# Kernel tuning notes

Measured on AMD Instinct MI355X. Metric: run time of the kernel, lower is better.

The kernel has to match this reference:

```python
import jax, jax.numpy as jnp
import numpy as np

NUM_BANDS = 12
D_MODEL = 128
NUM_HEADS = 2
HEAD_DIM = D_MODEL // NUM_HEADS


def setup_inputs() -> dict:
    key = jax.random.key(0)
    ks = jax.random.split(key, 12)
    d, B = D_MODEL, NUM_BANDS
    return {
        "x": jax.random.normal(ks[0], (4, 128, 128, B), dtype=jnp.float32),
        "w_embed": jax.random.normal(ks[1], (d,), dtype=jnp.float32) * 0.05,
        "b_embed": jax.random.normal(ks[2], (d,), dtype=jnp.float32) * 0.05,
        "band_pos": jax.random.normal(ks[3], (B, d), dtype=jnp.float32) * 0.02,
        "Wq": jax.random.normal(ks[4], (d, d), dtype=jnp.float32) * (1.0 / np.sqrt(d)),
        "bq": jax.random.normal(ks[5], (d,), dtype=jnp.float32) * 0.02,
        "Wk": jax.random.normal(ks[6], (d, d), dtype=jnp.float32) * (1.0 / np.sqrt(d)),
        "bk": jax.random.normal(ks[7], (d,), dtype=jnp.float32) * 0.02,
        "Wv": jax.random.normal(ks[8], (d, d), dtype=jnp.float32) * (1.0 / np.sqrt(d)),
        "bv": jax.random.normal(ks[9], (d,), dtype=jnp.float32) * 0.02,
        # out_proj is zero-init in the module; use tiny random values so the
        # output is numerically non-trivial for kernel correctness checks.
        "Wo": jax.random.normal(ks[10], (1, d), dtype=jnp.float32) * 0.02,
        "bo": jax.random.normal(ks[11], (1,), dtype=jnp.float32) * 0.02,
    }


def reference(x, w_embed, b_embed, band_pos, Wq, bq, Wk, bk, Wv, bv, Wo, bo):
    shape = x.shape
    x_flat = x.reshape(-1, NUM_BANDS)  # [N, B]
    N = x_flat.shape[0]
    H, hd = NUM_HEADS, HEAD_DIM
    # band_embed (Linear(1, d)) + band identity embedding -> tokens [N, B, d]
    tokens = x_flat[..., None] * w_embed + b_embed + band_pos
    # QKV projections, split heads
    Q = (tokens @ Wq.T + bq).reshape(N, NUM_BANDS, H, hd)
    K = (tokens @ Wk.T + bk).reshape(N, NUM_BANDS, H, hd)
    V = (tokens @ Wv.T + bv).reshape(N, NUM_BANDS, H, hd)
    scale = 1.0 / np.sqrt(hd).astype(np.float32)
    attn = jnp.einsum("nqhd,nkhd->nhqk", Q, K) * scale  # [N, H, B, B]
    attn = jax.nn.softmax(attn, axis=-1)
    out = jnp.einsum("nhqk,nkhd->nqhd", attn, V).reshape(N, NUM_BANDS, D_MODEL)
    delta = (out @ Wo.T + bo)[..., 0]  # out_proj -> [N, B]
    return (x_flat + delta).reshape(shape)
```

## Files before the change

### kernel.cpp

```cpp
#include <hip/hip_runtime.h>

#define D_MODEL 128
#define NBANDS 12
#define NHEADS 2
#define HDIM 64
#define NCONSTS 364
#define NROWS (39 * D_MODEL)
#define LOGIT_SCALE 0.18033688011112042f

__global__ __launch_bounds__(256) void spectral_inter_kernel(
    const float* __restrict__ w_embed, const float* __restrict__ b_embed,
    const float* __restrict__ band_pos,
    const float* __restrict__ Wq, const float* __restrict__ bq,
    const float* __restrict__ Wk, const float* __restrict__ bk,
    const float* __restrict__ Wv, const float* __restrict__ bv,
    float* __restrict__ inter)
{
    const int g    = (blockIdx.x * 256 + threadIdx.x) >> 6;
    const int lane = threadIdx.x & 63;
    const int mc   = g >> 7;
    const int row  = g & 127;
    const int m = mc / 13, c = mc % 13;
    const float* M    = (m == 0) ? Wq : (m == 1) ? Wk : Wv;
    const float* bias = (m == 0) ? bq : (m == 1) ? bk : bv;

    const float2 mv = reinterpret_cast<const float2*>(M + row * D_MODEL)[lane];
    float2 vv;
    if (c == 0) {
        vv = reinterpret_cast<const float2*>(w_embed)[lane];
    } else {
        float2 be = reinterpret_cast<const float2*>(b_embed)[lane];
        float2 bp = reinterpret_cast<const float2*>(band_pos + (c - 1) * D_MODEL)[lane];
        vv = make_float2(be.x + bp.x, be.y + bp.y);
    }
    float s = fmaf(mv.x, vv.x, mv.y * vv.y);
    #pragma unroll
    for (int off = 32; off; off >>= 1) s += __shfl_xor(s, off, 64);
    if (lane == 0) {
        if (c) s += bias[row];
        inter[g] = s;
    }
}

__global__ __launch_bounds__(384) void spectral_consts_kernel(
    const float* __restrict__ inter, const float* __restrict__ Wo,
    float* __restrict__ consts)
{
    __shared__ float si[NROWS];
    __shared__ float swo[D_MODEL];
    const int t = threadIdx.x;
    for (int i = t; i < NROWS; i += 384) si[i] = inter[i];
    if (t < D_MODEL) swo[t] = Wo[t];
    __syncthreads();

    const int idx = t;
    if (idx >= NCONSTS) return;
    const float* qv = si;
    const float* kv = si + 13 * D_MODEL;
    const float* vv = si + 26 * D_MODEL;

    float s = 0.f;
    if (idx < 2) {
        int h = idx;
        #pragma unroll 8
        for (int d = 0; d < HDIM; ++d) s = fmaf(qv[h*HDIM+d], kv[h*HDIM+d], s);
        s *= LOGIT_SCALE;
    } else if (idx < 4) {
        int h = idx - 2;
        #pragma unroll 8
        for (int d = 0; d < HDIM; ++d) s = fmaf(vv[h*HDIM+d], swo[h*HDIM+d], s);
    } else if (idx < 28) {
        int i = idx - 4, h = i / NBANDS, k = i % NBANDS;
        const float* kc = kv + (1 + k) * D_MODEL;
        #pragma unroll 8
        for (int d = 0; d < HDIM; ++d) s = fmaf(qv[h*HDIM+d], kc[h*HDIM+d], s);
        s *= LOGIT_SCALE;
    } else if (idx < 52) {
        int i = idx - 28, h = i / NBANDS, q = i % NBANDS;
        const float* qc = qv + (1 + q) * D_MODEL;
        #pragma unroll 8
        for (int d = 0; d < HDIM; ++d) s = fmaf(qc[h*HDIM+d], kv[h*HDIM+d], s);
        s *= LOGIT_SCALE;
    } else if (idx < 76) {
        int i = idx - 52, h = i / NBANDS, k = i % NBANDS;
        const float* vc = vv + (1 + k) * D_MODEL;
        #pragma unroll 8
        for (int d = 0; d < HDIM; ++d) s = fmaf(vc[h*HDIM+d], swo[h*HDIM+d], s);
    } else {
        int i = idx - 76, h = i / (NBANDS*NBANDS);
        int q = (i / NBANDS) % NBANDS, k = i % NBANDS;
        const float* qc = qv + (1 + q) * D_MODEL;
        const float* kc = kv + (1 + k) * D_MODEL;
        #pragma unroll 8
        for (int d = 0; d < HDIM; ++d) s = fmaf(qc[h*HDIM+d], kc[h*HDIM+d], s);
        s *= LOGIT_SCALE;
    }
    consts[idx] = s;
}

__global__ __launch_bounds__(256) void spectral_main_kernel(
    const float* __restrict__ x, const float* __restrict__ bo,
    const float* __restrict__ consts, float* __restrict__ out, int n_total)
{
    __shared__ float sc[NCONSTS];
    const int t = threadIdx.x;
    for (int i = t; i < NCONSTS; i += 256) sc[i] = consts[i];
    __syncthreads();

    const int tid = blockIdx.x * 256 + t;
    if (tid >= n_total) return;

    const unsigned n = (unsigned)tid / 12u;
    const int q = tid - (int)n * 12;

    const float4* xin = reinterpret_cast<const float4*>(x + (size_t)n * NBANDS);
    float4 p0 = xin[0], p1 = xin[1], p2 = xin[2];
    float xb[NBANDS] = {p0.x,p0.y,p0.z,p0.w, p1.x,p1.y,p1.z,p1.w, p2.x,p2.y,p2.z,p2.w};
    const float xq = x[tid];

    float acc = bo[0];
    #pragma unroll
    for (int h = 0; h < NHEADS; ++h) {
        const float a = sc[h];
        const float e = sc[2 + h];
        const float* u  = &sc[4  + h * NBANDS];
        const float vq  = sc[28 + h * NBANDS + q];
        const float* g  = &sc[52 + h * NBANDS];
        const float* wq = &sc[76 + h * NBANDS * NBANDS + q * NBANDS];
        const float coef = fmaf(a, xq, vq);
        float den = 0.f, num = 0.f;
        #pragma unroll
        for (int k = 0; k < NBANDS; ++k) {
            float sv = fmaf(coef, xb[k], fmaf(u[k], xq, wq[k]));
            float p  = __builtin_amdgcn_exp2f(sv);
            den += p;
            num  = fmaf(p, fmaf(e, xb[k], g[k]), num);
        }
        acc = fmaf(num, __builtin_amdgcn_rcpf(den), acc);
    }

    out[tid] = xq + acc;
}

extern "C" void kernel_launch(void* const* d_in, const int* in_sizes, int n_in,
                              void* d_out, int out_size, void* d_ws, size_t ws_size,
                              hipStream_t stream)
{
    const float* x  = (const float*)d_in[0];
    const float* we = (const float*)d_in[1];
    const float* be = (const float*)d_in[2];
    const float* bp = (const float*)d_in[3];
    const float* Wq = (const float*)d_in[4];
    const float* bq = (const float*)d_in[5];
    const float* Wk = (const float*)d_in[6];
    const float* bk = (const float*)d_in[7];
    const float* Wv = (const float*)d_in[8];
    const float* bv = (const float*)d_in[9];
    const float* Wo = (const float*)d_in[10];
    const float* bo = (const float*)d_in[11];
    float* out    = (float*)d_out;
    float* inter  = (float*)d_ws;
    float* consts = (float*)d_ws + NROWS;

    const int n_total = in_sizes[0];

    hipLaunchKernelGGL(spectral_inter_kernel, dim3(NROWS / 4), dim3(256), 0, stream,
                       we, be, bp, Wq, bq, Wk, bk, Wv, bv, inter);
    hipLaunchKernelGGL(spectral_consts_kernel, dim3(1), dim3(384), 0, stream,
                       inter, Wo, consts);
    hipLaunchKernelGGL(spectral_main_kernel,
                       dim3((n_total + 255) / 256), dim3(256), 0, stream,
                       x, bo, consts, out, n_total);
}
```

Before: 92.26 us.

## Fuse three kernels into one cooperative kernel with grid syncs

Replaces the three-launch pipeline (projection rows, constants, main attention) with a single cooperative kernel that uses grid-wide syncs between phases and grid-stride loops in the main phase. The constants phase becomes wave-parallel, with one wave reducing each dot product by shuffles instead of one thread looping serially in a single block. This aims to remove launch gaps and the serial single-block constants stage. In exchange it adds two grid barriers and caps the grid at 1024 blocks, and it falls back to the old path if the cooperative launch fails.

```diff
diff --git a/kernel.cpp b/kernel.cpp
--- a/kernel.cpp
+++ b/kernel.cpp
@@ -1,4 +1,7 @@
 #include <hip/hip_runtime.h>
+#include <hip/hip_cooperative_groups.h>
+
+namespace cg = cooperative_groups;
 
 #define D_MODEL 128
 #define NBANDS 12
@@ -6,7 +9,135 @@
 #define HDIM 64
 #define NCONSTS 364
 #define NROWS (39 * D_MODEL)
+#define BLOCK 256
 #define LOGIT_SCALE 0.18033688011112042f
+
+__global__ __launch_bounds__(BLOCK, 4) void spectral_fused_kernel(
+    const float* __restrict__ x,
+    const float* __restrict__ w_embed, const float* __restrict__ b_embed,
+    const float* __restrict__ band_pos,
+    const float* __restrict__ Wq, const float* __restrict__ bq,
+    const float* __restrict__ Wk, const float* __restrict__ bk,
+    const float* __restrict__ Wv, const float* __restrict__ bv,
+    const float* __restrict__ Wo, const float* __restrict__ bo,
+    float* __restrict__ ws, float* __restrict__ out, int n_total)
+{
+    const int t      = threadIdx.x;
+    const int lane   = t & 63;
+    const int bwave  = t >> 6;
+    const int nwaves = (int)(gridDim.x << 2);
+    const int gwave0 = (int)(blockIdx.x << 2) + bwave;
+
+    float* inter  = ws;
+    float* consts = ws + NROWS;
+
+    for (int g = gwave0; g < NROWS; g += nwaves) {
+        const int mc  = g >> 7;
+        const int row = g & 127;
+        const int m = mc / 13, c = mc - m * 13;
+        const float* M    = (m == 0) ? Wq : (m == 1) ? Wk : Wv;
+        const float* bias = (m == 0) ? bq : (m == 1) ? bk : bv;
+
+        const float2 mv = reinterpret_cast<const float2*>(M + row * D_MODEL)[lane];
+        float2 vv;
+        if (c == 0) {
+            vv = reinterpret_cast<const float2*>(w_embed)[lane];
+        } else {
+            const float2 be2 = reinterpret_cast<const float2*>(b_embed)[lane];
+            const float2 bp2 = reinterpret_cast<const float2*>(band_pos + (c - 1) * D_MODEL)[lane];
+            vv = make_float2(be2.x + bp2.x, be2.y + bp2.y);
+        }
+        float s = fmaf(mv.x, vv.x, mv.y * vv.y);
+        #pragma unroll
+        for (int off = 32; off; off >>= 1) s += __shfl_xor(s, off, 64);
+        if (lane == 0) inter[g] = c ? (s + bias[row]) : s;
+    }
+
+    __threadfence();
+    cg::this_grid().sync();
+
+    {
+        const float* qv = inter;
+        const float* kv = inter + 13 * D_MODEL;
+        const float* vv = inter + 26 * D_MODEL;
+        for (int idx = gwave0; idx < NCONSTS; idx += nwaves) {
+            float pa, pb, scale = LOGIT_SCALE;
+            if (idx < 2) {
+                pa = qv[idx * HDIM + lane];
+                pb = kv[idx * HDIM + lane];
+            } else if (idx < 4) {
+                const int h = idx - 2;
+                pa = vv[h * HDIM + lane];
+                pb = Wo[h * HDIM + lane];
+                scale = 1.f;
+            } else if (idx < 28) {
+                const int i = idx - 4, h = i / NBANDS, k = i - h * NBANDS;
+                pa = qv[h * HDIM + lane];
+                pb = kv[(1 + k) * D_MODEL + h * HDIM + lane];
+            } else if (idx < 52) {
+                const int i = idx - 28, h = i / NBANDS, q = i - h * NBANDS;
+                pa = qv[(1 + q) * D_MODEL + h * HDIM + lane];
+                pb = kv[h * HDIM + lane];
+            } else if (idx < 76) {
+                const int i = idx - 52, h = i / NBANDS, k = i - h * NBANDS;
+                pa = vv[(1 + k) * D_MODEL + h * HDIM + lane];
+                pb = Wo[h * HDIM + lane];
+                scale = 1.f;
+            } else {
+                const int i = idx - 76, h = i / (NBANDS * NBANDS);
+                const int r = i - h * NBANDS * NBANDS;
+                const int q = r / NBANDS, k = r - q * NBANDS;
+                pa = qv[(1 + q) * D_MODEL + h * HDIM + lane];
+                pb = kv[(1 + k) * D_MODEL + h * HDIM + lane];
+            }
+            float s = pa * pb;
+            #pragma unroll
+            for (int off = 32; off; off >>= 1) s += __shfl_xor(s, off, 64);
+            if (lane == 0) consts[idx] = s * scale;
+        }
+    }
+
+    __threadfence();
+    cg::this_grid().sync();
+
+    __shared__ float sc[NCONSTS];
+    for (int i = t; i < NCONSTS; i += BLOCK) sc[i] = consts[i];
+    __syncthreads();
+
+    const float bo0   = bo[0];
+    const int stride  = (int)gridDim.x * BLOCK;
+    for (int tid = (int)blockIdx.x * BLOCK + t; tid < n_total; tid += stride) {
+        const unsigned n = (unsigned)tid / 12u;
+        const int q = tid - (int)n * 12;
+
+        const float4* xin = reinterpret_cast<const float4*>(x + (size_t)n * NBANDS);
+        const float4 p0 = xin[0], p1 = xin[1], p2 = xin[2];
+        const float xb[NBANDS] = {p0.x,p0.y,p0.z,p0.w, p1.x,p1.y,p1.z,p1.w, p2.x,p2.y,p2.z,p2.w};
+        const float xq = x[tid];
+
+        float acc = bo0;
+        #pragma unroll
+        for (int h = 0; h < NHEADS; ++h) {
+            const float a = sc[h];
+            const float e = sc[2 + h];
+            const float* u  = &sc[4  + h * NBANDS];
+            const float vq  = sc[28 + h * NBANDS + q];
+            const float* g  = &sc[52 + h * NBANDS];
+            const float* wq = &sc[76 + h * NBANDS * NBANDS + q * NBANDS];
+            const float coef = fmaf(a, xq, vq);
+            float den = 0.f, num = 0.f;
+            #pragma unroll
+            for (int k = 0; k < NBANDS; ++k) {
+                const float sv = fmaf(coef, xb[k], fmaf(u[k], xq, wq[k]));
+                const float p  = __builtin_amdgcn_exp2f(sv);
+                den += p;
+                num  = fmaf(p, fmaf(e, xb[k], g[k]), num);
+            }
+            acc = fmaf(num, __builtin_amdgcn_rcpf(den), acc);
+        }
+        out[tid] = xq + acc;
+    }
+}
 
 __global__ __launch_bounds__(256) void spectral_inter_kernel(
     const float* __restrict__ w_embed, const float* __restrict__ b_embed,
@@ -159,16 +290,50 @@
     const float* Wo = (const float*)d_in[10];
     const float* bo = (const float*)d_in[11];
     float* out    = (float*)d_out;
-    float* inter  = (float*)d_ws;
-    float* consts = (float*)d_ws + NROWS;
-
-    const int n_total = in_sizes[0];
-
-    hipLaunchKernelGGL(spectral_inter_kernel, dim3(NROWS / 4), dim3(256), 0, stream,
-                       we, be, bp, Wq, bq, Wk, bk, Wv, bv, inter);
-    hipLaunchKernelGGL(spectral_consts_kernel, dim3(1), dim3(384), 0, stream,
-                       inter, Wo, consts);
-    hipLaunchKernelGGL(spectral_main_kernel,
-                       dim3((n_total + 255) / 256), dim3(256), 0, stream,
-                       x, bo, consts, out, n_total);
-}
+    float* ws     = (float*)d_ws;
+
+    int n_total = in_sizes[0];
+
+    static int coop_grid = -2;
+    if (coop_grid == -2) {
+        int nb = 0;
+        hipError_t e = hipOccupancyMaxActiveBlocksPerMultiprocessor(
+            &nb, spectral_fused_kernel, BLOCK, 0);
+        if (e == hipSuccess && nb >= 1) {
+            long g = (long)nb * 256;
+            if (g > 1024) g = 1024;
+            coop_grid = (int)g;
+        } else {
+            coop_grid = 0;
+        }
+    }
+
+    bool launched = false;
+    if (coop_grid > 0) {
+        void* args[] = {
+            (void*)&x,  (void*)&we, (void*)&be, (void*)&bp,
+            (void*)&Wq, (void*)&bq, (void*)&Wk, (void*)&bk,
+            (void*)&Wv, (void*)&bv, (void*)&Wo, (void*)&bo,
+            (void*)&ws, (void*)&out, (void*)&n_total
+        };
+        hipError_t err = hipLaunchCooperativeKernel(
+            spectral_fused_kernel, dim3(coop_grid), dim3(BLOCK), args, 0, stream);
+        if (err == hipSuccess) {
+            launched = true;
+        } else {
+            coop_grid = 0;
+        }
+    }
+
+    if (!launched) {
+        float* inter  = ws;
+        float* consts = ws + NROWS;
+        hipLaunchKernelGGL(spectral_inter_kernel, dim3(NROWS / 4), dim3(256), 0, stream,
+                           we, be, bp, Wq, bq, Wk, bk, Wv, bv, inter);
+        hipLaunchKernelGGL(spectral_consts_kernel, dim3(1), dim3(384), 0, stream,
+                           inter, Wo, consts);
+        hipLaunchKernelGGL(spectral_main_kernel,
+                           dim3((n_total + 255) / 256), dim3(256), 0, stream,
+                           x, bo, consts, out, n_total);
+    }
+}
```

New measurement: 251.6 us. +172.7%, slower.

## Fuse consts computation into main kernel with grid-stride persistent blocks

Applied to the files above, without the earlier changes.

Removes the single-block consts kernel and its launch. Each main-kernel block now recomputes the 364 attention constants from the inter buffer in global memory into shared memory. The main kernel becomes a grid-stride loop over 512 blocks, so that redundant constant computation is spread over fewer blocks. The trade-off is repeated per-block dot products and L2 reads, plus less parallelism per element if 512 blocks is too few.

```diff
diff --git a/kernel.cpp b/kernel.cpp
--- a/kernel.cpp
+++ b/kernel.cpp
@@ -6,6 +6,7 @@
 #define HDIM 64
 #define NCONSTS 364
 #define NROWS (39 * D_MODEL)
+#define NBLK_MAIN 512
 #define LOGIT_SCALE 0.18033688011112042f
 
 __global__ __launch_bounds__(256) void spectral_inter_kernel(
@@ -42,104 +43,96 @@
     }
 }
 
-__global__ __launch_bounds__(384) void spectral_consts_kernel(
-    const float* __restrict__ inter, const float* __restrict__ Wo,
-    float* __restrict__ consts)
+__device__ __forceinline__ float dot64(const float* __restrict__ a,
+                                       const float* __restrict__ b)
 {
-    __shared__ float si[NROWS];
-    __shared__ float swo[D_MODEL];
-    const int t = threadIdx.x;
-    for (int i = t; i < NROWS; i += 384) si[i] = inter[i];
-    if (t < D_MODEL) swo[t] = Wo[t];
-    __syncthreads();
-
-    const int idx = t;
-    if (idx >= NCONSTS) return;
-    const float* qv = si;
-    const float* kv = si + 13 * D_MODEL;
-    const float* vv = si + 26 * D_MODEL;
-
+    const float2* a2 = reinterpret_cast<const float2*>(a);
+    const float2* b2 = reinterpret_cast<const float2*>(b);
     float s = 0.f;
-    if (idx < 2) {
-        int h = idx;
-        #pragma unroll 8
-        for (int d = 0; d < HDIM; ++d) s = fmaf(qv[h*HDIM+d], kv[h*HDIM+d], s);
-        s *= LOGIT_SCALE;
-    } else if (idx < 4) {
-        int h = idx - 2;
-        #pragma unroll 8
-        for (int d = 0; d < HDIM; ++d) s = fmaf(vv[h*HDIM+d], swo[h*HDIM+d], s);
-    } else if (idx < 28) {
-        int i = idx - 4, h = i / NBANDS, k = i % NBANDS;
-        const float* kc = kv + (1 + k) * D_MODEL;
-        #pragma unroll 8
-        for (int d = 0; d < HDIM; ++d) s = fmaf(qv[h*HDIM+d], kc[h*HDIM+d], s);
-        s *= LOGIT_SCALE;
-    } else if (idx < 52) {
-        int i = idx - 28, h = i / NBANDS, q = i % NBANDS;
-        const float* qc = qv + (1 + q) * D_MODEL;
-        #pragma unroll 8
-        for (int d = 0; d < HDIM; ++d) s = fmaf(qc[h*HDIM+d], kv[h*HDIM+d], s);
-        s *= LOGIT_SCALE;
-    } else if (idx < 76) {
-        int i = idx - 52, h = i / NBANDS, k = i % NBANDS;
-        const float* vc = vv + (1 + k) * D_MODEL;
-        #pragma unroll 8
-        for (int d = 0; d < HDIM; ++d) s = fmaf(vc[h*HDIM+d], swo[h*HDIM+d], s);
-    } else {
-        int i = idx - 76, h = i / (NBANDS*NBANDS);
-        int q = (i / NBANDS) % NBANDS, k = i % NBANDS;
-        const float* qc = qv + (1 + q) * D_MODEL;
-        const float* kc = kv + (1 + k) * D_MODEL;
-        #pragma unroll 8
-        for (int d = 0; d < HDIM; ++d) s = fmaf(qc[h*HDIM+d], kc[h*HDIM+d], s);
-        s *= LOGIT_SCALE;
+    #pragma unroll
+    for (int i = 0; i < 32; ++i) {
+        const float2 x = a2[i], y = b2[i];
+        s = fmaf(x.x, y.x, s);
+        s = fmaf(x.y, y.y, s);
     }
-    consts[idx] = s;
+    return s;
 }
 
 __global__ __launch_bounds__(256) void spectral_main_kernel(
+    const float* __restrict__ inter, const float* __restrict__ Wo,
     const float* __restrict__ x, const float* __restrict__ bo,
-    const float* __restrict__ consts, float* __restrict__ out, int n_total)
+    float* __restrict__ out, int n_total)
 {
     __shared__ float sc[NCONSTS];
     const int t = threadIdx.x;
-    for (int i = t; i < NCONSTS; i += 256) sc[i] = consts[i];
+
+    {
+        const float* qv = inter;
+        const float* kv = inter + 13 * D_MODEL;
+        const float* vv = inter + 26 * D_MODEL;
+        for (int idx = t; idx < NCONSTS; idx += 256) {
+            float s;
+            if (idx < 2) {
+                s = dot64(qv + idx * HDIM, kv + idx * HDIM) * LOGIT_SCALE;
+            } else if (idx < 4) {
+                const int h = idx - 2;
+                s = dot64(vv + h * HDIM, Wo + h * HDIM);
+            } else if (idx < 28) {
+                const int i = idx - 4, h = i / NBANDS, k = i - h * NBANDS;
+                s = dot64(qv + h * HDIM,
+                          kv + (1 + k) * D_MODEL + h * HDIM) * LOGIT_SCALE;
+            } else if (idx < 52) {
+                const int i = idx - 28, h = i / NBANDS, q = i - h * NBANDS;
+                s = dot64(qv + (1 + q) * D_MODEL + h * HDIM,
+                          kv + h * HDIM) * LOGIT_SCALE;
+            } else if (idx < 76) {
+                const int i = idx - 52, h = i / NBANDS, k = i - h * NBANDS;
+                s = dot64(vv + (1 + k) * D_MODEL + h * HDIM, Wo + h * HDIM);
+            } else {
+                const int i = idx - 76, h = i / (NBANDS * NBANDS);
+                const int r = i - h * NBANDS * NBANDS;
+                const int q = r / NBANDS, k = r - q * NBANDS;
+                s = dot64(qv + (1 + q) * D_MODEL + h * HDIM,
+                          kv + (1 + k) * D_MODEL + h * HDIM) * LOGIT_SCALE;
+            }
+            sc[idx] = s;
+        }
+    }
     __syncthreads();
 
-    const int tid = blockIdx.x * 256 + t;
-    if (tid >= n_total) return;
+    const float bo0  = bo[0];
+    const int stride = (int)gridDim.x * 256;
+    for (int tid = (int)blockIdx.x * 256 + t; tid < n_total; tid += stride) {
+        const unsigned n = (unsigned)tid / 12u;
+        const int q = tid - (int)n * 12;
 
-    const unsigned n = (unsigned)tid / 12u;
-    const int q = tid - (int)n * 12;
+        const float4* xin = reinterpret_cast<const float4*>(x + (size_t)n * NBANDS);
+        const float4 p0 = xin[0], p1 = xin[1], p2 = xin[2];
+        const float xb[NBANDS] = {p0.x,p0.y,p0.z,p0.w, p1.x,p1.y,p1.z,p1.w, p2.x,p2.y,p2.z,p2.w};
+        const float xq = x[tid];
 
-    const float4* xin = reinterpret_cast<const float4*>(x + (size_t)n * NBANDS);
-    float4 p0 = xin[0], p1 = xin[1], p2 = xin[2];
-    float xb[NBANDS] = {p0.x,p0.y,p0.z,p0.w, p1.x,p1.y,p1.z,p1.w, p2.x,p2.y,p2.z,p2.w};
-    const float xq = x[tid];
-
-    float acc = bo[0];
-    #pragma unroll
-    for (int h = 0; h < NHEADS; ++h) {
-        const float a = sc[h];
-        const float e = sc[2 + h];
-        const float* u  = &sc[4  + h * NBANDS];
-        const float vq  = sc[28 + h * NBANDS + q];
-        const float* g  = &sc[52 + h * NBANDS];
-        const float* wq = &sc[76 + h * NBANDS * NBANDS + q * NBANDS];
-        const float coef = fmaf(a, xq, vq);
-        float den = 0.f, num = 0.f;
+        float acc = bo0;
         #pragma unroll
-        for (int k = 0; k < NBANDS; ++k) {
-            float sv = fmaf(coef, xb[k], fmaf(u[k], xq, wq[k]));
-            float p  = __builtin_amdgcn_exp2f(sv);
-            den += p;
-            num  = fmaf(p, fmaf(e, xb[k], g[k]), num);
+        for (int h = 0; h < NHEADS; ++h) {
+            const float a = sc[h];
+            const float e = sc[2 + h];
+            const float* u  = &sc[4  + h * NBANDS];
+            const float vq  = sc[28 + h * NBANDS + q];
+            const float* g  = &sc[52 + h * NBANDS];
+            const float* wq = &sc[76 + h * NBANDS * NBANDS + q * NBANDS];
+            const float coef = fmaf(a, xq, vq);
+            float den = 0.f, num = 0.f;
+            #pragma unroll
+            for (int k = 0; k < NBANDS; ++k) {
+                const float sv = fmaf(coef, xb[k], fmaf(u[k], xq, wq[k]));
+                const float p  = __builtin_amdgcn_exp2f(sv);
+                den += p;
+                num  = fmaf(p, fmaf(e, xb[k], g[k]), num);
+            }
+            acc = fmaf(num, __builtin_amdgcn_rcpf(den), acc);
         }
-        acc = fmaf(num, __builtin_amdgcn_rcpf(den), acc);
+        out[tid] = xq + acc;
     }
-
-    out[tid] = xq + acc;
 }
 
 extern "C" void kernel_launch(void* const* d_in, const int* in_sizes, int n_in,
@@ -158,17 +151,13 @@
     const float* bv = (const float*)d_in[9];
     const float* Wo = (const float*)d_in[10];
     const float* bo = (const float*)d_in[11];
-    float* out    = (float*)d_out;
-    float* inter  = (float*)d_ws;
-    float* consts = (float*)d_ws + NROWS;
+    float* out   = (float*)d_out;
+    float* inter = (float*)d_ws;
 
     const int n_total = in_sizes[0];
 
     hipLaunchKernelGGL(spectral_inter_kernel, dim3(NROWS / 4), dim3(256), 0, stream,
                        we, be, bp, Wq, bq, Wk, bk, Wv, bv, inter);
-    hipLaunchKernelGGL(spectral_consts_kernel, dim3(1), dim3(384), 0, stream,
-                       inter, Wo, consts);
-    hipLaunchKernelGGL(spectral_main_kernel,
-                       dim3((n_total + 255) / 256), dim3(256), 0, stream,
-                       x, bo, consts, out, n_total);
+    hipLaunchKernelGGL(spectral_main_kernel, dim3(NBLK_MAIN), dim3(256), 0, stream,
+                       inter, Wo, x, bo, out, n_total);
 }
```

After: 93.84 us. Within noise of the previous version (+1.7%).
